# Kernel optimization log

Measured on AMD Instinct MI355X. Metric: run time of the kernel, lower is better.

Reference implementation:

```python
import jax, jax.numpy as jnp
import numpy as np

N_NODES = 50000
N_EDGES = 1600000
N_FEAT = 512
N_HID = 256
N_CLS = 64
K_HOPS = 10
ALPHA = 0.1


def setup_inputs() -> dict:
    key = jax.random.key(0)
    k1, k2, k3, k4 = jax.random.split(key, 4)
    x = jax.random.normal(k1, (N_NODES, N_FEAT), dtype=jnp.float32)
    edge_index = jax.random.randint(k2, (2, N_EDGES), 0, N_NODES, dtype=jnp.int64)
    W1 = jax.random.normal(k3, (N_HID, N_FEAT), dtype=jnp.float32) * (1.0 / np.sqrt(N_FEAT))
    W2 = jax.random.normal(k4, (N_CLS, N_HID), dtype=jnp.float32) * (1.0 / np.sqrt(N_HID))
    return {"x": x, "edge_index": edge_index, "W1": W1, "W2": W2}


def reference(x, edge_index, W1, W2):
    n = x.shape[0]
    # --- MLP encoder (eval mode: dropout is identity) ---
    hidden = jax.nn.relu(x @ W1.T)            # [N, n_hidden]
    out = hidden @ W2.T                        # [N, n_classes]

    # --- GCN normalization with self-loops (PyG gcn_norm defaults) ---
    loops = jnp.arange(n, dtype=edge_index.dtype)
    src = jnp.concatenate([edge_index[0], loops])  # [E+N]
    dst = jnp.concatenate([edge_index[1], loops])  # [E+N]
    deg = jax.ops.segment_sum(jnp.ones_like(src, dtype=out.dtype), dst, num_segments=n)
    dinv = jnp.where(deg > 0, jax.lax.rsqrt(deg), 0.0)
    norm = dinv[src] * dinv[dst]                   # [E+N]

    # --- APPNP: K hops of propagate + teleport blend ---
    h0 = out
    for _ in range(K_HOPS):
        msg = norm[:, None] * out[src]                         # gather [E+N, C]
        agg = jax.ops.segment_sum(msg, dst, num_segments=n)    # scatter-add [N, C]
        out = (1.0 - ALPHA) * agg + ALPHA * h0

    return jax.nn.log_softmax(out, axis=1)
```

## Files before the change

kernel.cpp:

```cpp
#include <hip/hip_runtime.h>
#include <hip/hip_bf16.h>
#include <cstdint>
#include <cstddef>

#define N_NODES 50000
#define N_EDGES 1600000
#define N_FEAT  512
#define N_HID   256
#define N_CLS   64
#define K_HOPS  10
#define NPAD    50016
#define DUMMY   N_NODES
#define P16(d) (((d) + 15) & ~15)
#define STAGE_CAP 256
#define HOP_GRID 3125

typedef __attribute__((ext_vector_type(4))) float f32x4;
typedef __attribute__((ext_vector_type(4))) int   i32x4;
typedef __attribute__((ext_vector_type(2))) unsigned int u32x2;
typedef __attribute__((ext_vector_type(4))) unsigned short u16x4;
typedef __attribute__((ext_vector_type(8))) short s16x8;

__device__ __forceinline__ ushort f2bf(float f) {
    uint32_t u = __float_as_uint(f);
    uint32_t r = (u + 0x7FFFu + ((u >> 16) & 1u)) >> 16;
    return (ushort)r;
}

__device__ __forceinline__ uint32_t cvtpk(float a, float b) {
    uint32_t r;
    asm("v_cvt_pk_bf16_f32 %0, %1, %2" : "=v"(r) : "v"(a), "v"(b));
    return r;
}

__device__ __forceinline__ f32x4 bf4_to_f32(u16x4 v) {
    f32x4 r;
    r[0] = __uint_as_float((uint32_t)v[0] << 16);
    r[1] = __uint_as_float((uint32_t)v[1] << 16);
    r[2] = __uint_as_float((uint32_t)v[2] << 16);
    r[3] = __uint_as_float((uint32_t)v[3] << 16);
    return r;
}

__global__ void xb_k(const float* __restrict__ X, const float* __restrict__ W1,
                     ushort* __restrict__ Xb, ushort* __restrict__ W1b) {
    const size_t NX = (size_t)N_NODES * N_FEAT;
    const size_t NW = (size_t)N_HID * N_FEAT;
    size_t i = ((size_t)blockIdx.x * 256 + threadIdx.x) * 8;
    if (i < NX) {
        const f32x4 a = *reinterpret_cast<const f32x4*>(X + i);
        const f32x4 b = *reinterpret_cast<const f32x4*>(X + i + 4);
        uint4 o;
        o.x = cvtpk(a[0], a[1]); o.y = cvtpk(a[2], a[3]);
        o.z = cvtpk(b[0], b[1]); o.w = cvtpk(b[2], b[3]);
        *reinterpret_cast<uint4*>(Xb + i) = o;
    } else {
        size_t j = i - NX;
        if (j < NW) {
            const f32x4 a = *reinterpret_cast<const f32x4*>(W1 + j);
            const f32x4 b = *reinterpret_cast<const f32x4*>(W1 + j + 4);
            uint4 o;
            o.x = cvtpk(a[0], a[1]); o.y = cvtpk(a[2], a[3]);
            o.z = cvtpk(b[0], b[1]); o.w = cvtpk(b[2], b[3]);
            *reinterpret_cast<uint4*>(W1b + j) = o;
        }
    }
}

__launch_bounds__(256)
__global__ void gemm1_k(const ushort* __restrict__ Xb, const ushort* __restrict__ W1b,
                        ushort* __restrict__ H) {
    __shared__ ushort sA[128 * 64];
    __shared__ ushort sB[128 * 64];
    const int m0 = blockIdx.x * 128;
    const int n0 = blockIdx.y * 128;
    const int t = threadIdx.x;
    const int wid = t >> 6, lane = t & 63;
    const int wr = wid >> 1, wc = wid & 1;
    const int lo = lane & 15, hi = lane >> 4;

    f32x4 acc[4][4] = {};

    for (int kt = 0; kt < N_FEAT; kt += 64) {
        #pragma unroll
        for (int p = 0; p < 4; ++p) {
            int idx = p * 256 + t;
            int row = idx >> 3, g = idx & 7;
            int grow = m0 + row; if (grow > N_NODES - 1) grow = N_NODES - 1;
            uint4 v = *reinterpret_cast<const uint4*>(Xb + (size_t)grow * N_FEAT + kt + g * 8);
            *reinterpret_cast<uint4*>(&sA[row * 64 + ((g ^ (row & 7)) << 3)]) = v;
        }
        #pragma unroll
        for (int p = 0; p < 4; ++p) {
            int idx = p * 256 + t;
            int row = idx >> 3, g = idx & 7;
            uint4 v = *reinterpret_cast<const uint4*>(W1b + (size_t)(n0 + row) * N_FEAT + kt + g * 8);
            *reinterpret_cast<uint4*>(&sB[row * 64 + ((g ^ (row & 7)) << 3)]) = v;
        }
        __syncthreads();
        #pragma unroll
        for (int kk = 0; kk < 2; ++kk) {
            const int g = kk * 4 + hi;
            s16x8 a[4], b[4];
            #pragma unroll
            for (int i = 0; i < 4; ++i) {
                int row = wr * 64 + i * 16 + lo;
                a[i] = *reinterpret_cast<const s16x8*>(&sA[row * 64 + ((g ^ (row & 7)) << 3)]);
            }
            #pragma unroll
            for (int j = 0; j < 4; ++j) {
                int row = wc * 64 + j * 16 + lo;
                b[j] = *reinterpret_cast<const s16x8*>(&sB[row * 64 + ((g ^ (row & 7)) << 3)]);
            }
            #pragma unroll
            for (int i = 0; i < 4; ++i)
                #pragma unroll
                for (int j = 0; j < 4; ++j)
                    acc[i][j] = __builtin_amdgcn_mfma_f32_16x16x32_bf16(a[i], b[j], acc[i][j], 0, 0, 0);
        }
        __syncthreads();
    }
    #pragma unroll
    for (int i = 0; i < 4; ++i) {
        int rbase = m0 + wr * 64 + i * 16 + hi * 4;
        #pragma unroll
        for (int j = 0; j < 4; ++j) {
            int col = n0 + wc * 64 + j * 16 + lo;
            #pragma unroll
            for (int r = 0; r < 4; ++r) {
                int row = rbase + r;
                if (row < N_NODES) {
                    float v = acc[i][j][r];
                    H[(size_t)row * N_HID + col] = f2bf(fmaxf(v, 0.0f));
                }
            }
        }
    }
}

__launch_bounds__(256)
__global__ void gemm2_k(const ushort* __restrict__ H, const float* __restrict__ W2,
                        const float* __restrict__ dinv, ushort* __restrict__ out) {
    __shared__ ushort sA[128 * 64];
    __shared__ ushort sB[64 * 64];
    const int m0 = blockIdx.x * 128;
    const int t = threadIdx.x;
    const int wid = t >> 6, lane = t & 63;
    const int lo = lane & 15, hi = lane >> 4;

    f32x4 acc[2][4] = {};

    for (int kt = 0; kt < N_HID; kt += 64) {
        #pragma unroll
        for (int p = 0; p < 4; ++p) {
            int idx = p * 256 + t;
            int row = idx >> 3, g = idx & 7;
            int grow = m0 + row; if (grow > N_NODES - 1) grow = N_NODES - 1;
            uint4 v = *reinterpret_cast<const uint4*>(H + (size_t)grow * N_HID + kt + g * 8);
            *reinterpret_cast<uint4*>(&sA[row * 64 + ((g ^ (row & 7)) << 3)]) = v;
        }
        #pragma unroll
        for (int p = 0; p < 4; ++p) {
            int idx = p * 256 + t;
            int row = idx >> 4, f4 = idx & 15;
            const float4 v = *reinterpret_cast<const float4*>(W2 + (size_t)row * N_HID + kt + f4 * 4);
            uint2 h; h.x = cvtpk(v.x, v.y); h.y = cvtpk(v.z, v.w);
            int g = f4 >> 1;
            int off = row * 64 + ((g ^ (row & 7)) << 3) + ((f4 & 1) << 2);
            *reinterpret_cast<uint2*>(&sB[off]) = h;
        }
        __syncthreads();
        #pragma unroll
        for (int kk = 0; kk < 2; ++kk) {
            const int g = kk * 4 + hi;
            s16x8 a[2], b[4];
            #pragma unroll
            for (int i = 0; i < 2; ++i) {
                int row = wid * 32 + i * 16 + lo;
                a[i] = *reinterpret_cast<const s16x8*>(&sA[row * 64 + ((g ^ (row & 7)) << 3)]);
            }
            #pragma unroll
            for (int j = 0; j < 4; ++j) {
                int row = j * 16 + lo;
                b[j] = *reinterpret_cast<const s16x8*>(&sB[row * 64 + ((g ^ (row & 7)) << 3)]);
            }
            #pragma unroll
            for (int i = 0; i < 2; ++i)
                #pragma unroll
                for (int j = 0; j < 4; ++j)
                    acc[i][j] = __builtin_amdgcn_mfma_f32_16x16x32_bf16(a[i], b[j], acc[i][j], 0, 0, 0);
        }
        __syncthreads();
    }
    #pragma unroll
    for (int i = 0; i < 2; ++i) {
        int rbase = m0 + wid * 32 + i * 16 + hi * 4;
        #pragma unroll
        for (int r = 0; r < 4; ++r) {
            int row = rbase + r;
            if (row < N_NODES) {
                const float dv = dinv[row];
                #pragma unroll
                for (int j = 0; j < 4; ++j)
                    out[(size_t)row * 64 + j * 16 + lo] = f2bf(acc[i][j][r] * dv);
            }
        }
    }
}

__global__ void deg_k(const int* __restrict__ dst, int* __restrict__ deg,
                      int* __restrict__ pos) {
    int e = (blockIdx.x * 256 + threadIdx.x) * 4;
    if (e + 3 < N_EDGES) {
        const i32x4 d = __builtin_nontemporal_load(
            reinterpret_cast<const i32x4*>(dst + e));
        i32x4 p;
        p[0] = atomicAdd(&deg[d[0]], 1);
        p[1] = atomicAdd(&deg[d[1]], 1);
        p[2] = atomicAdd(&deg[d[2]], 1);
        p[3] = atomicAdd(&deg[d[3]], 1);
        __builtin_nontemporal_store(p, reinterpret_cast<i32x4*>(pos + e));
    } else {
        for (int k = 0; k < 4 && e + k < N_EDGES; ++k)
            pos[e + k] = atomicAdd(&deg[dst[e + k]], 1);
    }
}

__global__ void dinv_k(const int* __restrict__ deg, float* __restrict__ dinv,
                       float* __restrict__ rd) {
    int n = blockIdx.x * 256 + threadIdx.x;
    if (n < N_NODES) {
        float dp1 = (float)deg[n] + 1.0f;
        dinv[n] = rsqrtf(dp1);
        rd[n]   = sqrtf(dp1);
    }
}

__device__ __forceinline__ int wave_incl_scan(int v, int lane) {
    #pragma unroll
    for (int d = 1; d < 64; d <<= 1) {
        int u = __shfl_up(v, d, 64);
        if (lane >= d) v += u;
    }
    return v;
}

__global__ void scan_p1(const int* __restrict__ cnt, int* __restrict__ partial) {
    int i = blockIdx.x * 256 + threadIdx.x;
    int v = (i < N_NODES) ? P16(cnt[i]) : 0;
    #pragma unroll
    for (int d = 32; d; d >>= 1) v += __shfl_xor(v, d, 64);
    __shared__ int wt[4];
    int wid = threadIdx.x >> 6, lane = threadIdx.x & 63;
    if (lane == 0) wt[wid] = v;
    __syncthreads();
    if (threadIdx.x == 0) partial[blockIdx.x] = wt[0] + wt[1] + wt[2] + wt[3];
}

__global__ void scan_p2(const int* __restrict__ partial, int* __restrict__ chunkoff,
                        int* __restrict__ row_ptr) {
    int t = threadIdx.x;
    int v = (t < 196) ? partial[t] : 0;
    int lane = t & 63, wid = t >> 6;
    int incl = wave_incl_scan(v, lane);
    __shared__ int wt[4];
    if (lane == 63) wt[wid] = incl;
    __syncthreads();
    int woff = 0;
    for (int w = 0; w < wid; ++w) woff += wt[w];
    int excl = incl - v + woff;
    if (t < 196) chunkoff[t] = excl;
    if (t == 0) row_ptr[N_NODES] = wt[0] + wt[1] + wt[2] + wt[3];
}

__global__ void scan_p3(const int* __restrict__ cnt, const int* __restrict__ chunkoff,
                        int* __restrict__ row_ptr) {
    int i = blockIdx.x * 256 + threadIdx.x;
    int v = (i < N_NODES) ? P16(cnt[i]) : 0;
    int lane = threadIdx.x & 63, wid = threadIdx.x >> 6;
    int incl = wave_incl_scan(v, lane);
    __shared__ int wt[4];
    if (lane == 63) wt[wid] = incl;
    __syncthreads();
    int woff = 0;
    for (int w = 0; w < wid; ++w) woff += wt[w];
    int excl = incl - v + woff;
    if (i < N_NODES) row_ptr[i] = chunkoff[blockIdx.x] + excl;
}

__global__ void scatter_k(const int* __restrict__ src, const int* __restrict__ dst,
                          const int* __restrict__ pos, const int* __restrict__ row_ptr,
                          int* __restrict__ csr) {
    int e = (blockIdx.x * 256 + threadIdx.x) * 4;
    if (e + 3 < N_EDGES) {
        const i32x4 d4 = __builtin_nontemporal_load(
            reinterpret_cast<const i32x4*>(dst + e));
        const i32x4 s4 = __builtin_nontemporal_load(
            reinterpret_cast<const i32x4*>(src + e));
        const i32x4 p4 = __builtin_nontemporal_load(
            reinterpret_cast<const i32x4*>(pos + e));
        #pragma unroll
        for (int k = 0; k < 4; ++k)
            csr[row_ptr[d4[k]] + p4[k]] = s4[k];
    } else {
        for (int k = 0; k < 4 && e + k < N_EDGES; ++k)
            csr[row_ptr[dst[e + k]] + pos[e + k]] = src[e + k];
    }
}

__global__ void padfill_k(const int* __restrict__ deg, const int* __restrict__ row_ptr,
                          int* __restrict__ csr) {
    int n = blockIdx.x * 256 + threadIdx.x;
    if (n >= N_NODES) return;
    int d = deg[n];
    int base = row_ptr[n] + d;
    int pad = P16(d) - d;
    for (int i = 0; i < pad; ++i) csr[base + i] = DUMMY;
}

__global__ void zdum_k(ushort* __restrict__ b0, ushort* __restrict__ b1,
                       ushort* __restrict__ b2) {
    int t = threadIdx.x;
    if (t >= 192) return;
    ushort* b = (t < 64) ? b0 : (t < 128) ? b1 : b2;
    int w = t & 63;
    b[(size_t)DUMMY * 64 + w] = 0;
}

__launch_bounds__(256)
__global__ void hop_k(const ushort* __restrict__ prev, const ushort* __restrict__ h0,
                      ushort* __restrict__ next, const int* __restrict__ csr,
                      const int* __restrict__ row_ptr, const float* __restrict__ dinv) {
    __shared__ int scsr[4][STAGE_CAP];
    const int bid = blockIdx.x;
    const int wid = threadIdx.x >> 6;
    const int lane = threadIdx.x & 63;
    const int nb = bid * 16 + wid * 4;
    const int slot = lane >> 4;
    const int cq = (lane & 15) << 2;

    const int b0 = __builtin_amdgcn_readfirstlane(row_ptr[nb]);
    const int e0 = __builtin_amdgcn_readfirstlane(row_ptr[nb + 1]);
    const int e1 = __builtin_amdgcn_readfirstlane(row_ptr[nb + 2]);
    const int e2 = __builtin_amdgcn_readfirstlane(row_ptr[nb + 3]);
    const int e3 = __builtin_amdgcn_readfirstlane(row_ptr[nb + 4]);
    const int tot = e3 - b0;

    int* sw = scsr[wid];
    #pragma unroll
    for (int k = 0; k < 4; ++k) {
        int off = k * 64 + lane;
        if (off < tot && off < STAGE_CAP)
            sw[off] = __builtin_nontemporal_load(csr + b0 + off);
    }

    f32x4 a0 = {0.f,0.f,0.f,0.f}, a1 = a0, a2 = a0, a3 = a0;

#define NODE_LOOP(Bg, Eg, ACC)                                                   \
    {                                                                            \
        int ib = (Bg);                                                           \
        for (; ib + 32 <= (Eg); ib += 32) {                                      \
            int s[8];                                                            \
            if (ib + 32 - b0 <= STAGE_CAP) {                                     \
                int base = ib - b0 + slot;                                       \
                _Pragma("unroll")                                                \
                for (int k = 0; k < 8; ++k) s[k] = sw[base + 4 * k];             \
            } else {                                                             \
                _Pragma("unroll")                                                \
                for (int k = 0; k < 8; ++k)                                      \
                    s[k] = __builtin_nontemporal_load(csr + ib + slot + 4 * k);  \
            }                                                                    \
            u16x4 p[8];                                                          \
            _Pragma("unroll")                                                    \
            for (int k = 0; k < 8; ++k)                                          \
                p[k] = *reinterpret_cast<const u16x4*>(prev + (size_t)s[k] * 64 + cq); \
            _Pragma("unroll")                                                    \
            for (int k = 0; k < 8; ++k) {                                        \
                const f32x4 f = bf4_to_f32(p[k]);                                \
                ACC[0] += f[0]; ACC[1] += f[1]; ACC[2] += f[2]; ACC[3] += f[3];  \
            }                                                                    \
        }                                                                        \
        if (ib < (Eg)) {                                                         \
            int s[4];                                                            \
            if (ib + 16 - b0 <= STAGE_CAP) {                                     \
                int base = ib - b0 + slot;                                       \
                _Pragma("unroll")                                                \
                for (int k = 0; k < 4; ++k) s[k] = sw[base + 4 * k];             \
            } else {                                                             \
                _Pragma("unroll")                                                \
                for (int k = 0; k < 4; ++k)                                      \
                    s[k] = __builtin_nontemporal_load(csr + ib + slot + 4 * k);  \
            }                                                                    \
            u16x4 p[4];                                                          \
            _Pragma("unroll")                                                    \
            for (int k = 0; k < 4; ++k)                                          \
                p[k] = *reinterpret_cast<const u16x4*>(prev + (size_t)s[k] * 64 + cq); \
            _Pragma("unroll")                                                    \
            for (int k = 0; k < 4; ++k) {                                        \
                const f32x4 f = bf4_to_f32(p[k]);                                \
                ACC[0] += f[0]; ACC[1] += f[1]; ACC[2] += f[2]; ACC[3] += f[3];  \
            }                                                                    \
        }                                                                        \
    }

    NODE_LOOP(b0, e0, a0)
    NODE_LOOP(e0, e1, a1)
    NODE_LOOP(e1, e2, a2)
    NODE_LOOP(e2, e3, a3)
#undef NODE_LOOP

    #pragma unroll
    for (int c = 0; c < 4; ++c) {
        a0[c] += __shfl_xor(a0[c], 16, 64); a0[c] += __shfl_xor(a0[c], 32, 64);
        a1[c] += __shfl_xor(a1[c], 16, 64); a1[c] += __shfl_xor(a1[c], 32, 64);
        a2[c] += __shfl_xor(a2[c], 16, 64); a2[c] += __shfl_xor(a2[c], 32, 64);
        a3[c] += __shfl_xor(a3[c], 16, 64); a3[c] += __shfl_xor(a3[c], 32, 64);
    }

    {
        const int node = nb + slot;
        const float di = dinv[node];
        const float di2 = di * di;
        f32x4 av = a0;
        if (slot == 1) av = a1;
        if (slot == 2) av = a2;
        if (slot == 3) av = a3;
        const size_t off = (size_t)node * 64 + cq;
        const f32x4 pv = bf4_to_f32(*reinterpret_cast<const u16x4*>(prev + off));
        const f32x4 hh = bf4_to_f32(__builtin_nontemporal_load(
            reinterpret_cast<const u16x4*>(h0 + off)));
        float r0 = 0.9f * di2 * (av[0] + pv[0]) + 0.1f * hh[0];
        float r1 = 0.9f * di2 * (av[1] + pv[1]) + 0.1f * hh[1];
        float r2 = 0.9f * di2 * (av[2] + pv[2]) + 0.1f * hh[2];
        float r3 = 0.9f * di2 * (av[3] + pv[3]) + 0.1f * hh[3];
        u32x2 o;
        o[0] = cvtpk(r0, r1);
        o[1] = cvtpk(r2, r3);
        __builtin_nontemporal_store(o, reinterpret_cast<u32x2*>(next + off));
    }
}

__launch_bounds__(256)
__global__ void logsm_k(const ushort* __restrict__ in, const float* __restrict__ rd,
                        float* __restrict__ out) {
    int r = (blockIdx.x * 256 + threadIdx.x) >> 6;
    int lane = threadIdx.x & 63;
    if (r >= N_NODES) return;
    float v = __uint_as_float((uint32_t)in[(size_t)r * 64 + lane] << 16) * rd[r];
    float m = v;
    #pragma unroll
    for (int d = 32; d; d >>= 1) m = fmaxf(m, __shfl_xor(m, d, 64));
    float e = __expf(v - m);
    float s = e;
    #pragma unroll
    for (int d = 32; d; d >>= 1) s += __shfl_xor(s, d, 64);
    out[(size_t)r * N_CLS + lane] = (v - m) - __logf(s);
}

extern "C" void kernel_launch(void* const* d_in, const int* in_sizes, int n_in,
                              void* d_out, int out_size, void* d_ws, size_t ws_size,
                              hipStream_t stream) {
    const float* X  = (const float*)d_in[0];
    const int*   EI = (const int*)d_in[1];
    const float* W1 = (const float*)d_in[2];
    const float* W2 = (const float*)d_in[3];
    const int* src = EI;
    const int* dst = EI + N_EDGES;

    char* ws = (char*)d_ws;
    ushort* Xb     = (ushort*)(ws + 0);
    ushort* W1b    = (ushort*)(ws + 51200000);
    ushort* H      = (ushort*)(ws + 51462144);
    ushort* h0t    = (ushort*)(ws + 0);
    ushort* pp0    = (ushort*)(ws + 6402048);
    ushort* pp1    = (ushort*)(ws + 12804096);
    int*    csr    = (int*)  (ws + 19206144);
    int*    deg    = (int*)  (ws + 28806144);
    float*  dinv   = (float*)(ws + 29006144);
    float*  rd     = (float*)(ws + 29206144);
    int*    rptr   = (int*)  (ws + 29406144);
    int*    part   = (int*)  (ws + 29606148);
    int*    coff   = (int*)  (ws + 29606932);
    int*    pos    = (int*)  (ws + 29607744);

    xb_k<<<12564, 256, 0, stream>>>(X, W1, Xb, W1b);
    gemm1_k<<<dim3(391, 2), 256, 0, stream>>>(Xb, W1b, H);

    hipMemsetAsync(deg, 0, N_NODES * sizeof(int), stream);
    deg_k<<<1563, 256, 0, stream>>>(dst, deg, pos);
    dinv_k<<<196, 256, 0, stream>>>(deg, dinv, rd);
    scan_p1<<<196, 256, 0, stream>>>(deg, part);
    scan_p2<<<1, 256, 0, stream>>>(part, coff, rptr);
    scan_p3<<<196, 256, 0, stream>>>(deg, coff, rptr);
    scatter_k<<<1563, 256, 0, stream>>>(src, dst, pos, rptr, csr);
    padfill_k<<<196, 256, 0, stream>>>(deg, rptr, csr);

    gemm2_k<<<391, 256, 0, stream>>>(H, W2, dinv, h0t);
    zdum_k<<<1, 256, 0, stream>>>(h0t, pp0, pp1);

    const ushort* p = h0t;
    ushort* bufs[2] = {pp0, pp1};
    for (int k = 0; k < K_HOPS; ++k) {
        ushort* nx = bufs[k & 1];
        hop_k<<<HOP_GRID, 256, 0, stream>>>(p, h0t, nx, csr, rptr, dinv);
        p = nx;
    }
    logsm_k<<<12500, 256, 0, stream>>>(p, rd, (float*)d_out);
}
```

Before: 452.3 us.

## Fuse preprocessing kernels into GEMMs and drop separate bf16 conversion pass

Removes the standalone fp32-to-bf16 conversion kernel by converting X and W1 inside the first GEMM's shared-memory load. The degree-counting atomics now run as extra blocks of the GEMM1 launch, and the CSR scatter runs as extra blocks of the GEMM2 launch. The scan and pad-fill stages are merged into fewer kernels as well. Together this cuts launch count and avoids writing and re-reading a 51MB bf16 copy of X, at the cost of GEMM1 reading fp32 (twice the bytes per tile) and heterogeneous blocks sharing a launch.

```diff
diff --git a/kernel.cpp b/kernel.cpp
--- a/kernel.cpp
+++ b/kernel.cpp
@@ -14,6 +14,10 @@
 #define P16(d) (((d) + 15) & ~15)
 #define STAGE_CAP 256
 #define HOP_GRID 3125
+#define G1_BLOCKS 782
+#define DEG_BLOCKS 1563
+#define G2_BLOCKS 391
+#define SCAT_BLOCKS 1563
 
 typedef __attribute__((ext_vector_type(4))) float f32x4;
 typedef __attribute__((ext_vector_type(4))) int   i32x4;
@@ -42,39 +46,35 @@
     return r;
 }
 
-__global__ void xb_k(const float* __restrict__ X, const float* __restrict__ W1,
-                     ushort* __restrict__ Xb, ushort* __restrict__ W1b) {
-    const size_t NX = (size_t)N_NODES * N_FEAT;
-    const size_t NW = (size_t)N_HID * N_FEAT;
-    size_t i = ((size_t)blockIdx.x * 256 + threadIdx.x) * 8;
-    if (i < NX) {
-        const f32x4 a = *reinterpret_cast<const f32x4*>(X + i);
-        const f32x4 b = *reinterpret_cast<const f32x4*>(X + i + 4);
-        uint4 o;
-        o.x = cvtpk(a[0], a[1]); o.y = cvtpk(a[2], a[3]);
-        o.z = cvtpk(b[0], b[1]); o.w = cvtpk(b[2], b[3]);
-        *reinterpret_cast<uint4*>(Xb + i) = o;
-    } else {
-        size_t j = i - NX;
-        if (j < NW) {
-            const f32x4 a = *reinterpret_cast<const f32x4*>(W1 + j);
-            const f32x4 b = *reinterpret_cast<const f32x4*>(W1 + j + 4);
-            uint4 o;
-            o.x = cvtpk(a[0], a[1]); o.y = cvtpk(a[2], a[3]);
-            o.z = cvtpk(b[0], b[1]); o.w = cvtpk(b[2], b[3]);
-            *reinterpret_cast<uint4*>(W1b + j) = o;
-        }
-    }
-}
-
 __launch_bounds__(256)
-__global__ void gemm1_k(const ushort* __restrict__ Xb, const ushort* __restrict__ W1b,
-                        ushort* __restrict__ H) {
+__global__ void g1deg_k(const float* __restrict__ X, const float* __restrict__ W1,
+                        ushort* __restrict__ H, const int* __restrict__ dst,
+                        int* __restrict__ deg, int* __restrict__ pos) {
     __shared__ ushort sA[128 * 64];
     __shared__ ushort sB[128 * 64];
-    const int m0 = blockIdx.x * 128;
-    const int n0 = blockIdx.y * 128;
+    const int bid = blockIdx.x;
     const int t = threadIdx.x;
+
+    if (bid >= G1_BLOCKS) {
+        int e = ((bid - G1_BLOCKS) * 256 + t) * 4;
+        if (e + 3 < N_EDGES) {
+            const i32x4 d = __builtin_nontemporal_load(
+                reinterpret_cast<const i32x4*>(dst + e));
+            i32x4 p;
+            p[0] = atomicAdd(&deg[d[0]], 1);
+            p[1] = atomicAdd(&deg[d[1]], 1);
+            p[2] = atomicAdd(&deg[d[2]], 1);
+            p[3] = atomicAdd(&deg[d[3]], 1);
+            __builtin_nontemporal_store(p, reinterpret_cast<i32x4*>(pos + e));
+        } else {
+            for (int k = 0; k < 4 && e + k < N_EDGES; ++k)
+                pos[e + k] = atomicAdd(&deg[dst[e + k]], 1);
+        }
+        return;
+    }
+
+    const int m0 = (bid >> 1) * 128;
+    const int n0 = (bid & 1) * 128;
     const int wid = t >> 6, lane = t & 63;
     const int wr = wid >> 1, wc = wid & 1;
     const int lo = lane & 15, hi = lane >> 4;
@@ -83,19 +83,25 @@
 
     for (int kt = 0; kt < N_FEAT; kt += 64) {
         #pragma unroll
-        for (int p = 0; p < 4; ++p) {
+        for (int p = 0; p < 8; ++p) {
             int idx = p * 256 + t;
-            int row = idx >> 3, g = idx & 7;
+            int row = idx >> 4, f4 = idx & 15;
             int grow = m0 + row; if (grow > N_NODES - 1) grow = N_NODES - 1;
-            uint4 v = *reinterpret_cast<const uint4*>(Xb + (size_t)grow * N_FEAT + kt + g * 8);
-            *reinterpret_cast<uint4*>(&sA[row * 64 + ((g ^ (row & 7)) << 3)]) = v;
-        }
-        #pragma unroll
-        for (int p = 0; p < 4; ++p) {
+            const float4 v = *reinterpret_cast<const float4*>(X + (size_t)grow * N_FEAT + kt + f4 * 4);
+            uint2 h; h.x = cvtpk(v.x, v.y); h.y = cvtpk(v.z, v.w);
+            int g = f4 >> 1;
+            int off = row * 64 + ((g ^ (row & 7)) << 3) + ((f4 & 1) << 2);
+            *reinterpret_cast<uint2*>(&sA[off]) = h;
+        }
+        #pragma unroll
+        for (int p = 0; p < 8; ++p) {
             int idx = p * 256 + t;
-            int row = idx >> 3, g = idx & 7;
-            uint4 v = *reinterpret_cast<const uint4*>(W1b + (size_t)(n0 + row) * N_FEAT + kt + g * 8);
-            *reinterpret_cast<uint4*>(&sB[row * 64 + ((g ^ (row & 7)) << 3)]) = v;
+            int row = idx >> 4, f4 = idx & 15;
+            const float4 v = *reinterpret_cast<const float4*>(W1 + (size_t)(n0 + row) * N_FEAT + kt + f4 * 4);
+            uint2 h; h.x = cvtpk(v.x, v.y); h.y = cvtpk(v.z, v.w);
+            int g = f4 >> 1;
+            int off = row * 64 + ((g ^ (row & 7)) << 3) + ((f4 & 1) << 2);
+            *reinterpret_cast<uint2*>(&sB[off]) = h;
         }
         __syncthreads();
         #pragma unroll
@@ -138,104 +144,6 @@
     }
 }
 
-__launch_bounds__(256)
-__global__ void gemm2_k(const ushort* __restrict__ H, const float* __restrict__ W2,
-                        const float* __restrict__ dinv, ushort* __restrict__ out) {
-    __shared__ ushort sA[128 * 64];
-    __shared__ ushort sB[64 * 64];
-    const int m0 = blockIdx.x * 128;
-    const int t = threadIdx.x;
-    const int wid = t >> 6, lane = t & 63;
-    const int lo = lane & 15, hi = lane >> 4;
-
-    f32x4 acc[2][4] = {};
-
-    for (int kt = 0; kt < N_HID; kt += 64) {
-        #pragma unroll
-        for (int p = 0; p < 4; ++p) {
-            int idx = p * 256 + t;
-            int row = idx >> 3, g = idx & 7;
-            int grow = m0 + row; if (grow > N_NODES - 1) grow = N_NODES - 1;
-            uint4 v = *reinterpret_cast<const uint4*>(H + (size_t)grow * N_HID + kt + g * 8);
-            *reinterpret_cast<uint4*>(&sA[row * 64 + ((g ^ (row & 7)) << 3)]) = v;
-        }
-        #pragma unroll
-        for (int p = 0; p < 4; ++p) {
-            int idx = p * 256 + t;
-            int row = idx >> 4, f4 = idx & 15;
-            const float4 v = *reinterpret_cast<const float4*>(W2 + (size_t)row * N_HID + kt + f4 * 4);
-            uint2 h; h.x = cvtpk(v.x, v.y); h.y = cvtpk(v.z, v.w);
-            int g = f4 >> 1;
-            int off = row * 64 + ((g ^ (row & 7)) << 3) + ((f4 & 1) << 2);
-            *reinterpret_cast<uint2*>(&sB[off]) = h;
-        }
-        __syncthreads();
-        #pragma unroll
-        for (int kk = 0; kk < 2; ++kk) {
-            const int g = kk * 4 + hi;
-            s16x8 a[2], b[4];
-            #pragma unroll
-            for (int i = 0; i < 2; ++i) {
-                int row = wid * 32 + i * 16 + lo;
-                a[i] = *reinterpret_cast<const s16x8*>(&sA[row * 64 + ((g ^ (row & 7)) << 3)]);
-            }
-            #pragma unroll
-            for (int j = 0; j < 4; ++j) {
-                int row = j * 16 + lo;
-                b[j] = *reinterpret_cast<const s16x8*>(&sB[row * 64 + ((g ^ (row & 7)) << 3)]);
-            }
-            #pragma unroll
-            for (int i = 0; i < 2; ++i)
-                #pragma unroll
-                for (int j = 0; j < 4; ++j)
-                    acc[i][j] = __builtin_amdgcn_mfma_f32_16x16x32_bf16(a[i], b[j], acc[i][j], 0, 0, 0);
-        }
-        __syncthreads();
-    }
-    #pragma unroll
-    for (int i = 0; i < 2; ++i) {
-        int rbase = m0 + wid * 32 + i * 16 + hi * 4;
-        #pragma unroll
-        for (int r = 0; r < 4; ++r) {
-            int row = rbase + r;
-            if (row < N_NODES) {
-                const float dv = dinv[row];
-                #pragma unroll
-                for (int j = 0; j < 4; ++j)
-                    out[(size_t)row * 64 + j * 16 + lo] = f2bf(acc[i][j][r] * dv);
-            }
-        }
-    }
-}
-
-__global__ void deg_k(const int* __restrict__ dst, int* __restrict__ deg,
-                      int* __restrict__ pos) {
-    int e = (blockIdx.x * 256 + threadIdx.x) * 4;
-    if (e + 3 < N_EDGES) {
-        const i32x4 d = __builtin_nontemporal_load(
-            reinterpret_cast<const i32x4*>(dst + e));
-        i32x4 p;
-        p[0] = atomicAdd(&deg[d[0]], 1);
-        p[1] = atomicAdd(&deg[d[1]], 1);
-        p[2] = atomicAdd(&deg[d[2]], 1);
-        p[3] = atomicAdd(&deg[d[3]], 1);
-        __builtin_nontemporal_store(p, reinterpret_cast<i32x4*>(pos + e));
-    } else {
-        for (int k = 0; k < 4 && e + k < N_EDGES; ++k)
-            pos[e + k] = atomicAdd(&deg[dst[e + k]], 1);
-    }
-}
-
-__global__ void dinv_k(const int* __restrict__ deg, float* __restrict__ dinv,
-                       float* __restrict__ rd) {
-    int n = blockIdx.x * 256 + threadIdx.x;
-    if (n < N_NODES) {
-        float dp1 = (float)deg[n] + 1.0f;
-        dinv[n] = rsqrtf(dp1);
-        rd[n]   = sqrtf(dp1);
-    }
-}
-
 __device__ __forceinline__ int wave_incl_scan(int v, int lane) {
     #pragma unroll
     for (int d = 1; d < 64; d <<= 1) {
@@ -245,11 +153,18 @@
     return v;
 }
 
-__global__ void scan_p1(const int* __restrict__ cnt, int* __restrict__ partial) {
+__global__ void dsc1_k(const int* __restrict__ deg, float* __restrict__ dinv,
+                       float* __restrict__ rd, int* __restrict__ partial) {
     int i = blockIdx.x * 256 + threadIdx.x;
-    int v = (i < N_NODES) ? P16(cnt[i]) : 0;
-    #pragma unroll
-    for (int d = 32; d; d >>= 1) v += __shfl_xor(v, d, 64);
+    int d = (i < N_NODES) ? deg[i] : 0;
+    if (i < N_NODES) {
+        float dp1 = (float)d + 1.0f;
+        dinv[i] = rsqrtf(dp1);
+        rd[i]   = sqrtf(dp1);
+    }
+    int v = (i < N_NODES) ? P16(d) : 0;
+    #pragma unroll
+    for (int s = 32; s; s >>= 1) v += __shfl_xor(v, s, 64);
     __shared__ int wt[4];
     int wid = threadIdx.x >> 6, lane = threadIdx.x & 63;
     if (lane == 0) wt[wid] = v;
@@ -257,8 +172,9 @@
     if (threadIdx.x == 0) partial[blockIdx.x] = wt[0] + wt[1] + wt[2] + wt[3];
 }
 
-__global__ void scan_p2(const int* __restrict__ partial, int* __restrict__ chunkoff,
-                        int* __restrict__ row_ptr) {
+__global__ void sc2_k(const int* __restrict__ partial, int* __restrict__ chunkoff,
+                      int* __restrict__ row_ptr, ushort* __restrict__ b0,
+                      ushort* __restrict__ b1, ushort* __restrict__ b2) {
     int t = threadIdx.x;
     int v = (t < 196) ? partial[t] : 0;
     int lane = t & 63, wid = t >> 6;
@@ -271,12 +187,17 @@
     int excl = incl - v + woff;
     if (t < 196) chunkoff[t] = excl;
     if (t == 0) row_ptr[N_NODES] = wt[0] + wt[1] + wt[2] + wt[3];
-}
-
-__global__ void scan_p3(const int* __restrict__ cnt, const int* __restrict__ chunkoff,
-                        int* __restrict__ row_ptr) {
+    if (t < 192) {
+        ushort* b = (t < 64) ? b0 : (t < 128) ? b1 : b2;
+        b[(size_t)DUMMY * 64 + (t & 63)] = 0;
+    }
+}
+
+__global__ void sc3_k(const int* __restrict__ cnt, const int* __restrict__ chunkoff,
+                      int* __restrict__ row_ptr, int* __restrict__ csr) {
     int i = blockIdx.x * 256 + threadIdx.x;
-    int v = (i < N_NODES) ? P16(cnt[i]) : 0;
+    int dg = (i < N_NODES) ? cnt[i] : 0;
+    int v = (i < N_NODES) ? P16(dg) : 0;
     int lane = threadIdx.x & 63, wid = threadIdx.x >> 6;
     int incl = wave_incl_scan(v, lane);
     __shared__ int wt[4];
@@ -285,46 +206,107 @@
     int woff = 0;
     for (int w = 0; w < wid; ++w) woff += wt[w];
     int excl = incl - v + woff;
-    if (i < N_NODES) row_ptr[i] = chunkoff[blockIdx.x] + excl;
-}
-
-__global__ void scatter_k(const int* __restrict__ src, const int* __restrict__ dst,
-                          const int* __restrict__ pos, const int* __restrict__ row_ptr,
-                          int* __restrict__ csr) {
-    int e = (blockIdx.x * 256 + threadIdx.x) * 4;
-    if (e + 3 < N_EDGES) {
-        const i32x4 d4 = __builtin_nontemporal_load(
-            reinterpret_cast<const i32x4*>(dst + e));
-        const i32x4 s4 = __builtin_nontemporal_load(
-            reinterpret_cast<const i32x4*>(src + e));
-        const i32x4 p4 = __builtin_nontemporal_load(
-            reinterpret_cast<const i32x4*>(pos + e));
-        #pragma unroll
-        for (int k = 0; k < 4; ++k)
-            csr[row_ptr[d4[k]] + p4[k]] = s4[k];
-    } else {
-        for (int k = 0; k < 4 && e + k < N_EDGES; ++k)
-            csr[row_ptr[dst[e + k]] + pos[e + k]] = src[e + k];
-    }
-}
-
-__global__ void padfill_k(const int* __restrict__ deg, const int* __restrict__ row_ptr,
-                          int* __restrict__ csr) {
-    int n = blockIdx.x * 256 + threadIdx.x;
-    if (n >= N_NODES) return;
-    int d = deg[n];
-    int base = row_ptr[n] + d;
-    int pad = P16(d) - d;
-    for (int i = 0; i < pad; ++i) csr[base + i] = DUMMY;
-}
-
-__global__ void zdum_k(ushort* __restrict__ b0, ushort* __restrict__ b1,
-                       ushort* __restrict__ b2) {
-    int t = threadIdx.x;
-    if (t >= 192) return;
-    ushort* b = (t < 64) ? b0 : (t < 128) ? b1 : b2;
-    int w = t & 63;
-    b[(size_t)DUMMY * 64 + w] = 0;
+    if (i < N_NODES) {
+        int rp = chunkoff[blockIdx.x] + excl;
+        row_ptr[i] = rp;
+        int base = rp + dg;
+        int pad = P16(dg) - dg;
+        for (int k = 0; k < pad; ++k) csr[base + k] = DUMMY;
+    }
+}
+
+__launch_bounds__(256)
+__global__ void scg2_k(const ushort* __restrict__ H, const float* __restrict__ W2,
+                       const float* __restrict__ dinv, ushort* __restrict__ out,
+                       const int* __restrict__ src, const int* __restrict__ dst,
+                       const int* __restrict__ pos, const int* __restrict__ row_ptr,
+                       int* __restrict__ csr) {
+    __shared__ ushort sA[128 * 64];
+    __shared__ ushort sB[64 * 64];
+    const int bid = blockIdx.x;
+    const int t = threadIdx.x;
+
+    if (bid >= G2_BLOCKS) {
+        int e = ((bid - G2_BLOCKS) * 256 + t) * 4;
+        if (e + 3 < N_EDGES) {
+            const i32x4 d4 = __builtin_nontemporal_load(
+                reinterpret_cast<const i32x4*>(dst + e));
+            const i32x4 s4 = __builtin_nontemporal_load(
+                reinterpret_cast<const i32x4*>(src + e));
+            const i32x4 p4 = __builtin_nontemporal_load(
+                reinterpret_cast<const i32x4*>(pos + e));
+            #pragma unroll
+            for (int k = 0; k < 4; ++k)
+                csr[row_ptr[d4[k]] + p4[k]] = s4[k];
+        } else {
+            for (int k = 0; k < 4 && e + k < N_EDGES; ++k)
+                csr[row_ptr[dst[e + k]] + pos[e + k]] = src[e + k];
+        }
+        return;
+    }
+
+    const int m0 = bid * 128;
+    const int wid = t >> 6, lane = t & 63;
+    const int lo = lane & 15, hi = lane >> 4;
+
+    f32x4 acc[2][4] = {};
+
+    for (int kt = 0; kt < N_HID; kt += 64) {
+        #pragma unroll
+        for (int p = 0; p < 4; ++p) {
+            int idx = p * 256 + t;
+            int row = idx >> 3, g = idx & 7;
+            int grow = m0 + row; if (grow > N_NODES - 1) grow = N_NODES - 1;
+            uint4 v = *reinterpret_cast<const uint4*>(H + (size_t)grow * N_HID + kt + g * 8);
+            *reinterpret_cast<uint4*>(&sA[row * 64 + ((g ^ (row & 7)) << 3)]) = v;
+        }
+        #pragma unroll
+        for (int p = 0; p < 4; ++p) {
+            int idx = p * 256 + t;
+            int row = idx >> 4, f4 = idx & 15;
+            const float4 v = *reinterpret_cast<const float4*>(W2 + (size_t)row * N_HID + kt + f4 * 4);
+            uint2 h; h.x = cvtpk(v.x, v.y); h.y = cvtpk(v.z, v.w);
+            int g = f4 >> 1;
+            int off = row * 64 + ((g ^ (row & 7)) << 3) + ((f4 & 1) << 2);
+            *reinterpret_cast<uint2*>(&sB[off]) = h;
+        }
+        __syncthreads();
+        #pragma unroll
+        for (int kk = 0; kk < 2; ++kk) {
+            const int g = kk * 4 + hi;
+            s16x8 a[2], b[4];
+            #pragma unroll
+            for (int i = 0; i < 2; ++i) {
+                int row = wid * 32 + i * 16 + lo;
+                a[i] = *reinterpret_cast<const s16x8*>(&sA[row * 64 + ((g ^ (row & 7)) << 3)]);
+            }
+            #pragma unroll
+            for (int j = 0; j < 4; ++j) {
+                int row = j * 16 + lo;
+                b[j] = *reinterpret_cast<const s16x8*>(&sB[row * 64 + ((g ^ (row & 7)) << 3)]);
+            }
+            #pragma unroll
+            for (int i = 0; i < 2; ++i)
+                #pragma unroll
+                for (int j = 0; j < 4; ++j)
+                    acc[i][j] = __builtin_amdgcn_mfma_f32_16x16x32_bf16(a[i], b[j], acc[i][j], 0, 0, 0);
+        }
+        __syncthreads();
+    }
+    #pragma unroll
+    for (int i = 0; i < 2; ++i) {
+        int rbase = m0 + wid * 32 + i * 16 + hi * 4;
+        #pragma unroll
+        for (int r = 0; r < 4; ++r) {
+            int row = rbase + r;
+            if (row < N_NODES) {
+                const float dv = dinv[row];
+                #pragma unroll
+                for (int j = 0; j < 4; ++j)
+                    out[(size_t)row * 64 + j * 16 + lo] = f2bf(acc[i][j][r] * dv);
+            }
+        }
+    }
 }
 
 __launch_bounds__(256)
@@ -468,35 +450,29 @@
     const int* dst = EI + N_EDGES;
 
     char* ws = (char*)d_ws;
-    ushort* Xb     = (ushort*)(ws + 0);
-    ushort* W1b    = (ushort*)(ws + 51200000);
-    ushort* H      = (ushort*)(ws + 51462144);
-    ushort* h0t    = (ushort*)(ws + 0);
-    ushort* pp0    = (ushort*)(ws + 6402048);
-    ushort* pp1    = (ushort*)(ws + 12804096);
-    int*    csr    = (int*)  (ws + 19206144);
-    int*    deg    = (int*)  (ws + 28806144);
-    float*  dinv   = (float*)(ws + 29006144);
-    float*  rd     = (float*)(ws + 29206144);
-    int*    rptr   = (int*)  (ws + 29406144);
-    int*    part   = (int*)  (ws + 29606148);
-    int*    coff   = (int*)  (ws + 29606932);
-    int*    pos    = (int*)  (ws + 29607744);
-
-    xb_k<<<12564, 256, 0, stream>>>(X, W1, Xb, W1b);
-    gemm1_k<<<dim3(391, 2), 256, 0, stream>>>(Xb, W1b, H);
+    ushort* H      = (ushort*)(ws + 0);
+    int*    csr    = (int*)  (ws + 25600000);
+    int*    deg    = (int*)  (ws + 35200000);
+    float*  dinv   = (float*)(ws + 35400000);
+    float*  rd     = (float*)(ws + 35600000);
+    int*    rptr   = (int*)  (ws + 35800000);
+    int*    part   = (int*)  (ws + 36000016);
+    int*    coff   = (int*)  (ws + 36001024);
+    int*    pos    = (int*)  (ws + 36002048);
+    ushort* h0t    = (ushort*)(ws + 42402048);
+    ushort* pp0    = (ushort*)(ws + 48804096);
+    ushort* pp1    = (ushort*)(ws + 55206144);
 
     hipMemsetAsync(deg, 0, N_NODES * sizeof(int), stream);
-    deg_k<<<1563, 256, 0, stream>>>(dst, deg, pos);
-    dinv_k<<<196, 256, 0, stream>>>(deg, dinv, rd);
-    scan_p1<<<196, 256, 0, stream>>>(deg, part);
-    scan_p2<<<1, 256, 0, stream>>>(part, coff, rptr);
-    scan_p3<<<196, 256, 0, stream>>>(deg, coff, rptr);
-    scatter_k<<<1563, 256, 0, stream>>>(src, dst, pos, rptr, csr);
-    padfill_k<<<196, 256, 0, stream>>>(deg, rptr, csr);
-
-    gemm2_k<<<391, 256, 0, stream>>>(H, W2, dinv, h0t);
-    zdum_k<<<1, 256, 0, stream>>>(h0t, pp0, pp1);
+
+    g1deg_k<<<G1_BLOCKS + DEG_BLOCKS, 256, 0, stream>>>(X, W1, H, dst, deg, pos);
+
+    dsc1_k<<<196, 256, 0, stream>>>(deg, dinv, rd, part);
+    sc2_k<<<1, 256, 0, stream>>>(part, coff, rptr, h0t, pp0, pp1);
+    sc3_k<<<196, 256, 0, stream>>>(deg, coff, rptr, csr);
+
+    scg2_k<<<G2_BLOCKS + SCAT_BLOCKS, 256, 0, stream>>>(H, W2, dinv, h0t,
+                                                        src, dst, pos, rptr, csr);
 
     const ushort* p = h0t;
     ushort* bufs[2] = {pp0, pp1};
```

Result: faster. 406.7 us, median of 3 (-10.1%).
